# Optimization experiments

Hardware: AMD Instinct MI355X
Metric: run time of the kernel (lower is better)

## Reference

```python
import jax, jax.numpy as jnp
import numpy as np

ALPHA = 0.2  # LeakyReLU negative slope from init kwarg
NEG_INF = -9e15


def gat_multihead(x, adj_mask, W, a, concat):
    """Standard (GLMP-style) dense GAT, all heads at once.
    x: [B,N,Din], adj_mask: [B,N,N] bool, W: [H,Din,F], a: [H,2F].
    """
    B, N, _ = x.shape
    H, _, F = W.shape
    Wh = jnp.einsum('bnd,hdf->bhnf', x, W)              # [B,H,N,F]
    f1 = jnp.einsum('bhnf,hf->bhn', Wh, a[:, :F])
    f2 = jnp.einsum('bhnf,hf->bhn', Wh, a[:, F:])
    e = jax.nn.leaky_relu(f1[:, :, :, None] + f2[:, :, None, :], ALPHA)  # [B,H,N,N]
    e = jnp.where(adj_mask[:, None], e, NEG_INF)
    att = jax.nn.softmax(e, axis=-1)
    out = jnp.einsum('bhij,bhjf->bhif', att, Wh)        # [B,H,N,F]
    if concat:
        out = jax.nn.elu(out)
        return out.transpose(0, 2, 1, 3).reshape(B, N, H * F)
    # concat=False heads are summed and divided by nheads in load_graph -> mean
    return out.mean(axis=1)


def setup_inputs() -> dict:
    key = jax.random.key(0)
    ks = jax.random.split(key, 12)
    B, N, T = 16, 1024, 6
    V, D, F, H = 32000, 128, 64, 4
    CONV_MAX = 400
    story = jax.random.randint(ks[0], (B, N, T), 0, V)
    kb_len = jax.random.randint(ks[1], (B,), 1, CONV_MAX)
    conv_len = jax.random.randint(ks[2], (B,), 1, CONV_MAX)
    hidden = jax.random.normal(ks[3], (B, F), dtype=jnp.float32)
    dh_outputs = jax.random.normal(ks[4], (B, CONV_MAX, D), dtype=jnp.float32)
    adj = (jax.random.uniform(ks[5], (B, N, N)) < 0.05).astype(jnp.float32)
    emb = jax.random.normal(ks[6], (V, D), dtype=jnp.float32) * 0.1
    W1 = jax.random.normal(ks[7], (H, D, F), dtype=jnp.float32) * 0.1
    a1 = jax.random.normal(ks[8], (H, 2 * F), dtype=jnp.float32) * 0.1
    W2 = jax.random.normal(ks[9], (H, H * F, F), dtype=jnp.float32) * 0.1
    a2 = jax.random.normal(ks[10], (H, 2 * F), dtype=jnp.float32) * 0.1
    W3 = jax.random.normal(ks[11], (H, H * F, F), dtype=jnp.float32) * 0.1
    a3 = jax.random.normal(jax.random.fold_in(key, 99), (H, 2 * F), dtype=jnp.float32) * 0.1
    return {"story": story, "kb_len": kb_len, "conv_len": conv_len,
            "hidden": hidden, "dh_outputs": dh_outputs, "adj": adj,
            "emb": emb, "W1": W1, "a1": a1, "W2": W2, "a2": a2, "W3": W3, "a3": a3}


def reference(story, kb_len, conv_len, hidden, dh_outputs, adj, emb, W1, a1, W2, a2, W3, a3):
    B, N, T = story.shape
    Lc = dh_outputs.shape[1]
    # Embedding lookup + bag-of-words sum over memory token slots
    x = emb[story].sum(axis=2)                              # [B,N,D]
    # add_lm_embedding: scatter dh_outputs[b, :conv_len[b]] into slots
    # [kb_len[b]-1, kb_len[b]-1+conv_len[b]) of the memory (vectorized)
    pos = jnp.arange(N)[None, :]                            # [1,N]
    off = pos - (kb_len[:, None] - 1)                       # [B,N]
    valid = (off >= 0) & (off < conv_len[:, None])
    idx = jnp.clip(off, 0, Lc - 1)
    gathered = jnp.take_along_axis(dh_outputs, idx[:, :, None], axis=1)  # [B,N,D]
    x = x + jnp.where(valid[:, :, None], gathered, 0.0)
    # update_pad_token_adj: self-loop for pad slots k >= kb_len+conv_len
    d = jnp.arange(N)
    start = kb_len + conv_len                               # (kb_len-1)+conv_len+1
    diag = adj[:, d, d]
    adj = adj.at[:, d, d].set(jnp.where(d[None, :] >= start[:, None], 1.0, diag))
    adj_mask = adj > 0
    # Three GAT stacks (dropout omitted: eval mode)
    x = gat_multihead(x, adj_mask, W1, a1, concat=True)     # [B,N,H*F]
    x = gat_multihead(x, adj_mask, W2, a2, concat=True)     # [B,N,H*F]
    x = jax.nn.sigmoid(gat_multihead(x, adj_mask, W3, a3, concat=False))  # [B,N,F]
    prob_logits = jnp.einsum('bnf,bf->bn', x, hidden)       # [B,N]
    return (jax.nn.sigmoid(prob_logits), hidden, prob_logits)
```

## Files before the change

### kernel.cpp

```cpp
#include <hip/hip_runtime.h>
#include <stdint.h>

typedef short bf16x8 __attribute__((ext_vector_type(8)));
typedef float f32x4 __attribute__((ext_vector_type(4)));
typedef unsigned short u16;
typedef unsigned short u16x4 __attribute__((ext_vector_type(4)));
typedef unsigned int u32;
typedef unsigned int u32x4 __attribute__((ext_vector_type(4)));
typedef unsigned long long u64;


__device__ inline u16 f2b(float f) {
    unsigned u = __float_as_uint(f);
    u += 0x7fffu + ((u >> 16) & 1u);
    return (u16)(u >> 16);
}

__device__ inline float wred_sum(float v) {
    #pragma unroll
    for (int m = 32; m >= 1; m >>= 1) v += __shfl_xor(v, m, 64);
    return v;
}

__global__ __launch_bounds__(256) void k_pre(const float* __restrict__ adj,
                                             const int* __restrict__ kb,
                                             const int* __restrict__ cv,
                                             const int* __restrict__ story,
                                             const float* __restrict__ dh,
                                             const float* __restrict__ emb,
                                             const float* __restrict__ W1,
                                             const float* __restrict__ a1,
                                             const float* __restrict__ W2,
                                             const float* __restrict__ a2,
                                             const float* __restrict__ W3,
                                             const float* __restrict__ a3,
                                             u64* __restrict__ mask,
                                             u16* __restrict__ x0,
                                             u16* __restrict__ Bp1,
                                             u16* __restrict__ Bp2,
                                             u16* __restrict__ Bp3,
                                             float* __restrict__ d0g) {
    int bid = blockIdx.x;
    int tid = threadIdx.x;
    if (bid < 1024) {
        int w = tid >> 6, l = tid & 63;
        int rbase = (bid << 4) + (w << 2);
        int b = rbase >> 10;
        int start = kb[b] + cv[b];
        const float4* a4 = (const float4*)adj;
        for (int r = 0; r < 4; ++r) {
            int row = rbase + r;
            int i = row & 1023;
            u32 m16 = 0;
            #pragma unroll
            for (int q = 0; q < 4; ++q) {
                float4 v = a4[(size_t)row * 256 + (l << 2) + q];
                m16 |= (u32)(v.x > 0.0f) << (q * 4);
                m16 |= (u32)(v.y > 0.0f) << (q * 4 + 1);
                m16 |= (u32)(v.z > 0.0f) << (q * 4 + 2);
                m16 |= (u32)(v.w > 0.0f) << (q * 4 + 3);
            }
            if (i >= start && (i >> 4) == l) m16 |= 1u << (i & 15);
            u64 bal = __ballot(m16 != 0);
            u32 s0 = (u32)__shfl((int)m16, (l << 2) + 0, 64);
            u32 s1 = (u32)__shfl((int)m16, (l << 2) + 1, 64);
            u32 s2 = (u32)__shfl((int)m16, (l << 2) + 2, 64);
            u32 s3 = (u32)__shfl((int)m16, (l << 2) + 3, 64);
            if (l < 16) {
                u64 word = (u64)(s0 | (s1 << 16)) | ((u64)(s2 | (s3 << 16)) << 32);
                mask[((size_t)row << 4) + l] = word;
            }
            if (l == 0) d0g[row] = (bal == 0ull) ? 1.0f : 0.0f;
        }
    } else if (bid < 3072) {
        int w = tid >> 6, l = tid & 63;
        int r = l >> 5, dq = l & 31;
        int bn = ((bid - 1024) << 3) + (w << 1) + r;
        int b = bn >> 10, n = bn & 1023;
        const int* st = story + (size_t)bn * 6;
        const float4* emb4 = (const float4*)emb;
        float4 acc = {0.f, 0.f, 0.f, 0.f};
        #pragma unroll
        for (int t = 0; t < 6; ++t) {
            int tok = st[t];
            float4 e = emb4[(size_t)tok * 32 + dq];
            acc.x += e.x; acc.y += e.y; acc.z += e.z; acc.w += e.w;
        }
        int off = n - (kb[b] - 1);
        if (off >= 0 && off < cv[b]) {
            float4 d = ((const float4*)dh)[((size_t)b * 400 + off) * 32 + dq];
            acc.x += d.x; acc.y += d.y; acc.z += d.z; acc.w += d.w;
        }
        u16x4 pk = {f2b(acc.x), f2b(acc.y), f2b(acc.z), f2b(acc.w)};
        *(u16x4*)(x0 + ((size_t)bn << 7) + (dq << 2)) = pk;
    } else {
        int pb = bid - 3072;
        const float *W, *a; u16* Bp; int K;
        if (pb < 136)      { W = W1; a = a1; Bp = Bp1; K = 128; }
        else if (pb < 408) { W = W2; a = a2; Bp = Bp2; K = 256; pb -= 136; }
        else               { W = W3; a = a3; Bp = Bp3; K = 256; pb -= 408; }
        int id = pb * 256 + tid;
        int j = id & 7, lane = (id >> 3) & 63, fr = id >> 9;
        int kt = fr / 17, ct = fr - kt * 17;
        int kk = (kt << 5) + ((lane >> 4) << 3) + j;
        u16 o;
        if (ct < 16) {
            int col = (ct << 4) | (lane & 15);
            o = f2b(W[((size_t)(col >> 6) * K + kk) * 64 + (col & 63)]);
        } else {
            int c = lane & 15;
            if (c < 8) {
                int h = c >> 1, wh = c & 1;
                const float4* wr = (const float4*)(W + ((size_t)h * K + kk) * 64);
                const float4* av = (const float4*)(a + h * 128 + wh * 64);
                float s = 0.0f;
                #pragma unroll
                for (int q = 0; q < 16; ++q) {
                    float4 x = wr[q], y = av[q];
                    s += x.x * y.x + x.y * y.y + x.z * y.z + x.w * y.w;
                }
                o = f2b(s);
            } else o = 0;
        }
        Bp[id] = o;
    }
}

template <int KT>
__global__ __launch_bounds__(256) void k_gemm(const u16* __restrict__ A,
                                              const u16* __restrict__ Bp,
                                              u16* __restrict__ WhB,
                                              float* __restrict__ f1,
                                              float* __restrict__ f2) {
    constexpr int K = KT * 32;
    __shared__ __align__(16) u16 tile[4][2][2048];
    int tid = threadIdx.x, w = tid >> 6, l = tid & 63;
    int rtp = blockIdx.x;
    int colq = w;
    int m0 = rtp << 5;
    int b = m0 >> 10, n0 = m0 & 1023;
    int jt = n0 >> 5;
    const bf16x8* Av = (const bf16x8*)A;
    const bf16x8* Bv = (const bf16x8*)Bp;
    int arowA = m0 + (l & 15);
    bf16x8 afA[KT], afB[KT];
    #pragma unroll
    for (int kt = 0; kt < KT; ++kt) {
        size_t base = ((size_t)arowA * K + (kt << 5) + ((l >> 4) << 3)) >> 3;
        afA[kt] = Av[base];
        afB[kt] = Av[base + ((16 * K) >> 3)];
    }
    f32x4 accA[4], accB[4];
    #pragma unroll
    for (int c = 0; c < 4; ++c) { accA[c] = f32x4{0.f,0.f,0.f,0.f}; accB[c] = f32x4{0.f,0.f,0.f,0.f}; }
    f32x4 acc16A = {0.f,0.f,0.f,0.f}, acc16B = {0.f,0.f,0.f,0.f};
    #pragma unroll
    for (int kt = 0; kt < KT; ++kt) {
        #pragma unroll
        for (int c = 0; c < 4; ++c) {
            bf16x8 bv = Bv[(size_t)(kt * 17 + (colq << 2) + c) * 64 + l];
            accA[c] = __builtin_amdgcn_mfma_f32_16x16x32_bf16(afA[kt], bv, accA[c], 0, 0, 0);
            accB[c] = __builtin_amdgcn_mfma_f32_16x16x32_bf16(afB[kt], bv, accB[c], 0, 0, 0);
        }
        if (colq == 0) {
            bf16x8 bv = Bv[(size_t)(kt * 17 + 16) * 64 + l];
            acc16A = __builtin_amdgcn_mfma_f32_16x16x32_bf16(afA[kt], bv, acc16A, 0, 0, 0);
            acc16B = __builtin_amdgcn_mfma_f32_16x16x32_bf16(afB[kt], bv, acc16B, 0, 0, 0);
        }
    }
    int co = l & 15, ro = (l >> 4) << 2;
    if (colq == 0 && co < 8) {
        int hh = co >> 1;
        float* fp = (co & 1) ? f2 : f1;
        int base = (((b << 2) + hh) << 10) + n0 + ro;
        #pragma unroll
        for (int r = 0; r < 4; ++r) {
            fp[base + r] = acc16A[r];
            fp[base + 16 + r] = acc16B[r];
        }
    }
    u16* twA = tile[w][0]; u16* twB = tile[w][1];
    #pragma unroll
    for (int c = 0; c < 4; ++c) {
        int col2 = (c << 4) + co;
        u16x4 pkA, pkB;
        #pragma unroll
        for (int r = 0; r < 4; ++r) { pkA[r] = f2b(accA[c][r]); pkB[r] = f2b(accB[c][r]); }
        *(u16x4*)(twA + (col2 << 4) + ro) = pkA;
        *(u16x4*)(twB + (col2 << 4) + ro) = pkB;
    }
    __syncthreads();
    int bh = (b << 2) + colq;
    int lq = l & 31;
    #pragma unroll
    for (int ftq = 0; ftq < 2; ++ftq) {
        int ft = (ftq << 1) + (l >> 5);
        int col2 = (ft << 4) + (l & 15);
        int r0 = ((l >> 4) & 1) << 3;
        bf16x8 vA = *(const bf16x8*)(twA + (col2 << 4) + r0);
        bf16x8 vB = *(const bf16x8*)(twB + (col2 << 4) + r0);
        size_t fidx = (size_t)((bh << 7) + (jt << 2) + ft);
        *(bf16x8*)(WhB + (fidx * 64 + lq) * 8) = vA;
        *(bf16x8*)(WhB + (fidx * 64 + 32 + lq) * 8) = vB;
    }
}

#define PV_CORE(f2v4, mw, f1i, d0f, fragbase, Bv, acc, accs, g)                  \
    {                                                                            \
        u32 onep = ((l & 15) == 0) ? 0x3F803F80u : 0u;                           \
        u32x4 ov = {onep, onep, onep, onep};                                     \
        bf16x8 sfrag = __builtin_bit_cast(bf16x8, ov);                           \
        for (int jt = 0; jt < 32; ++jt) {                                        \
            u32 sh = mw[jt] >> (g << 3);                                         \
            f32x4 fa = f2v4[(jt << 3) + (g << 1)];                               \
            f32x4 fb = f2v4[(jt << 3) + (g << 1) + 1];                           \
            float p[8];                                                          \
            _Pragma("unroll")                                                    \
            for (int jj = 0; jj < 8; ++jj) {                                     \
                float f2j = (jj < 4) ? fa[jj] : fb[jj - 4];                      \
                float t = f1i + f2j;                                             \
                float e = fmaxf(t, 0.2f * t);                                    \
                float ex;                                                        \
                asm("v_exp_f32 %0, %1" : "=v"(ex) : "v"(e));                     \
                p[jj] = (sh & (1u << jj)) ? ex : d0f;                            \
            }                                                                    \
            u32x4 pk;                                                            \
            _Pragma("unroll")                                                    \
            for (int q = 0; q < 4; ++q) {                                        \
                u32 r;                                                           \
                asm("v_cvt_pk_bf16_f32 %0, %1, %2"                               \
                    : "=v"(r) : "v"(p[2 * q]), "v"(p[2 * q + 1]));               \
                pk[q] = r;                                                       \
            }                                                                    \
            bf16x8 af = __builtin_bit_cast(bf16x8, pk);                          \
            accs = __builtin_amdgcn_mfma_f32_16x16x32_bf16(af, sfrag, accs, 0, 0, 0); \
            _Pragma("unroll")                                                    \
            for (int ft = 0; ft < 4; ++ft)                                       \
                acc[ft] = __builtin_amdgcn_mfma_f32_16x16x32_bf16(               \
                    af, Bv[(size_t)(fragbase + (jt << 2) + ft) * 64 + l], acc[ft], 0, 0, 0); \
        }                                                                        \
    }

__global__ __launch_bounds__(256) void k_pv0(const u32* __restrict__ mask32,
                                             const float* __restrict__ f1g,
                                             const float* __restrict__ f2g,
                                             const float* __restrict__ d0g,
                                             const bf16x8* __restrict__ Bv,
                                             u16* __restrict__ xout) {
    __shared__ __align__(16) float f2s[1024];
    const float LOG2E = 1.44269504088896340736f;
    int tid = threadIdx.x;
    int w = tid >> 6, l = tid & 63;
    int bh = blockIdx.x >> 4;
    int b = bh >> 2, h = bh & 3;
    int itile = ((blockIdx.x & 15) << 2) + w;
    int i0 = itile << 4;
    for (int idx = tid; idx < 1024; idx += 256) f2s[idx] = f2g[(bh << 10) + idx] * LOG2E;
    __syncthreads();
    int row = l & 15, g = l >> 4;
    int i = i0 + row;
    float f1i = f1g[(bh << 10) + i] * LOG2E;
    float d0f = d0g[(b << 10) + i];
    const u32x4* m4 = (const u32x4*)(mask32 + (((size_t)(b << 10) + i) << 5));
    u32 mw[32];
    #pragma unroll
    for (int t4 = 0; t4 < 8; ++t4) {
        u32x4 q = m4[t4];
        mw[t4 * 4 + 0] = q[0]; mw[t4 * 4 + 1] = q[1];
        mw[t4 * 4 + 2] = q[2]; mw[t4 * 4 + 3] = q[3];
    }
    f32x4 acc[4];
    #pragma unroll
    for (int ft = 0; ft < 4; ++ft) acc[ft] = f32x4{0.f, 0.f, 0.f, 0.f};
    f32x4 accs = {0.f, 0.f, 0.f, 0.f};
    const f32x4* f2v4 = (const f32x4*)f2s;
    int fragbase = bh << 7;
    PV_CORE(f2v4, mw, f1i, d0f, fragbase, Bv, acc, accs, g)
    #pragma unroll
    for (int reg = 0; reg < 4; ++reg) {
        int orow = (g << 2) + reg;
        float s = __shfl(accs[reg], g << 4, 64);
        float rinv = 1.0f / s;
        int grow = i0 + orow;
        #pragma unroll
        for (int ft = 0; ft < 4; ++ft) {
            float v = acc[ft][reg] * rinv;
            float e2 = v > 0.0f ? v : (__expf(v) - 1.0f);
            xout[((size_t)((b << 10) + grow) << 8) + (h << 6) + (ft << 4) + row] = f2b(e2);
        }
    }
}

__global__ __launch_bounds__(256) void k_pv3(const u32* __restrict__ mask32,
                                             const float* __restrict__ f1g,
                                             const float* __restrict__ f2g,
                                             const float* __restrict__ d0g,
                                             const bf16x8* __restrict__ Bv,
                                             const float* __restrict__ hidden,
                                             float* __restrict__ dout) {
    __shared__ __align__(16) float shbuf[4096];
    const float LOG2E = 1.44269504088896340736f;
    int tid = threadIdx.x;
    int w = tid >> 6, l = tid & 63;
    int b = blockIdx.x >> 6;
    int itile = blockIdx.x & 63;
    int i0 = itile << 4;
    int bh = (b << 2) + w;
    for (int idx = tid; idx < 4096; idx += 256) shbuf[idx] = f2g[(b << 12) + idx] * LOG2E;
    __syncthreads();
    int row = l & 15, g = l >> 4;
    int i = i0 + row;
    float f1i = f1g[(bh << 10) + i] * LOG2E;
    float d0f = d0g[(b << 10) + i];
    const u32x4* m4 = (const u32x4*)(mask32 + (((size_t)(b << 10) + i) << 5));
    u32 mw[32];
    #pragma unroll
    for (int t4 = 0; t4 < 8; ++t4) {
        u32x4 q = m4[t4];
        mw[t4 * 4 + 0] = q[0]; mw[t4 * 4 + 1] = q[1];
        mw[t4 * 4 + 2] = q[2]; mw[t4 * 4 + 3] = q[3];
    }
    f32x4 acc[4];
    #pragma unroll
    for (int ft = 0; ft < 4; ++ft) acc[ft] = f32x4{0.f, 0.f, 0.f, 0.f};
    f32x4 accs = {0.f, 0.f, 0.f, 0.f};
    const f32x4* f2v4 = (const f32x4*)(shbuf + (w << 10));
    int fragbase = bh << 7;
    PV_CORE(f2v4, mw, f1i, d0f, fragbase, Bv, acc, accs, g)
    __syncthreads();
    #pragma unroll
    for (int reg = 0; reg < 4; ++reg) {
        int orow = (g << 2) + reg;
        float s = __shfl(accs[reg], g << 4, 64);
        float rinv = 1.0f / s;
        #pragma unroll
        for (int ft = 0; ft < 4; ++ft)
            shbuf[(w << 10) + (orow << 6) + (ft << 4) + row] = acc[ft][reg] * rinv;
    }
    __syncthreads();
    float hid = hidden[(b << 6) + l];
    #pragma unroll
    for (int k = 0; k < 4; ++k) {
        int rl = (k << 2) + w;
        int o = (rl << 6) + l;
        float s = shbuf[o] + shbuf[1024 + o] + shbuf[2048 + o] + shbuf[3072 + o];
        s *= 0.25f;
        float x = 1.0f / (1.0f + __expf(-s));
        float logit = wred_sum(x * hid);
        if (l == 0) {
            int grow = i0 + rl;
            dout[(b << 10) + grow] = 1.0f / (1.0f + __expf(-logit));
            dout[17408 + (b << 10) + grow] = logit;
        }
    }
    if (itile == 0 && w == 0) dout[16384 + (b << 6) + l] = hid;
}

extern "C" void kernel_launch(void* const* d_in, const int* in_sizes, int n_in,
                              void* d_out, int out_size, void* d_ws, size_t ws_size,
                              hipStream_t stream) {
    const int*   story  = (const int*)d_in[0];
    const int*   kb     = (const int*)d_in[1];
    const int*   cv     = (const int*)d_in[2];
    const float* hidden = (const float*)d_in[3];
    const float* dh     = (const float*)d_in[4];
    const float* adj    = (const float*)d_in[5];
    const float* emb    = (const float*)d_in[6];
    const float* W1     = (const float*)d_in[7];
    const float* a1     = (const float*)d_in[8];
    const float* W2     = (const float*)d_in[9];
    const float* a2     = (const float*)d_in[10];
    const float* W3     = (const float*)d_in[11];
    const float* a3     = (const float*)d_in[12];
    float* dout = (float*)d_out;

    char* ws = (char*)d_ws;
    u64*   mask   = (u64*)(ws + 0);
    u32*   mask32 = (u32*)(ws + 0);
    u16*   x0   = (u16*)(ws + 2097152);
    u16*   xbf  = (u16*)(ws + 6291456);
    u16*   WhB  = (u16*)(ws + 14680064);
    float* f1   = (float*)(ws + 23068672);
    float* f2   = (float*)(ws + 23330816);
    u16*   Bp1  = (u16*)(ws + 23592960);
    u16*   Bp2  = (u16*)(ws + 23662592);
    u16*   Bp3  = (u16*)(ws + 23801856);
    float* d0g  = (float*)(ws + 23941120);

    k_pre<<<3752, 256, 0, stream>>>(adj, kb, cv, story, dh, emb,
                                    W1, a1, W2, a2, W3, a3,
                                    mask, x0, Bp1, Bp2, Bp3, d0g);

    k_gemm<4><<<512, 256, 0, stream>>>(x0, Bp1, WhB, f1, f2);
    k_pv0<<<1024, 256, 0, stream>>>(mask32, f1, f2, d0g, (const bf16x8*)WhB, xbf);

    k_gemm<8><<<512, 256, 0, stream>>>(xbf, Bp2, WhB, f1, f2);
    k_pv0<<<1024, 256, 0, stream>>>(mask32, f1, f2, d0g, (const bf16x8*)WhB, xbf);

    k_gemm<8><<<512, 256, 0, stream>>>(xbf, Bp3, WhB, f1, f2);
    k_pv3<<<1024, 256, 0, stream>>>(mask32, f1, f2, d0g, (const bf16x8*)WhB, hidden, dout);
}
```

Baseline: 151.5 us.

## Halve GEMM row tile and split final layer into PV plus reduction kernel

The projection GEMM now processes 16 rows per block instead of 32, doubling the grid to 1024 blocks and dropping the block-wide barrier. The last attention layer reuses the generic PV kernel to write per-head fp32 outputs to workspace, and a new kernel averages the heads, applies the sigmoid and computes the logits. The aim is more parallelism in the GEMM and a PV kernel that is lighter on shared memory and needs fewer barriers. The cost is an extra launch and an fp32 round-trip through global memory for the final layer, and each GEMM block now reloads the B fragments for half as many rows.

```diff
diff --git a/kernel.cpp b/kernel.cpp
--- a/kernel.cpp
+++ b/kernel.cpp
@@ -133,40 +133,33 @@
                                               float* __restrict__ f1,
                                               float* __restrict__ f2) {
     constexpr int K = KT * 32;
-    __shared__ __align__(16) u16 tile[4][2][2048];
+    __shared__ __align__(16) u16 tile[4][1024];
     int tid = threadIdx.x, w = tid >> 6, l = tid & 63;
-    int rtp = blockIdx.x;
     int colq = w;
-    int m0 = rtp << 5;
+    int m0 = blockIdx.x << 4;
     int b = m0 >> 10, n0 = m0 & 1023;
-    int jt = n0 >> 5;
+    int jt = n0 >> 5, halfsel = (n0 >> 4) & 1;
     const bf16x8* Av = (const bf16x8*)A;
     const bf16x8* Bv = (const bf16x8*)Bp;
-    int arowA = m0 + (l & 15);
-    bf16x8 afA[KT], afB[KT];
-    #pragma unroll
-    for (int kt = 0; kt < KT; ++kt) {
-        size_t base = ((size_t)arowA * K + (kt << 5) + ((l >> 4) << 3)) >> 3;
-        afA[kt] = Av[base];
-        afB[kt] = Av[base + ((16 * K) >> 3)];
-    }
-    f32x4 accA[4], accB[4];
-    #pragma unroll
-    for (int c = 0; c < 4; ++c) { accA[c] = f32x4{0.f,0.f,0.f,0.f}; accB[c] = f32x4{0.f,0.f,0.f,0.f}; }
-    f32x4 acc16A = {0.f,0.f,0.f,0.f}, acc16B = {0.f,0.f,0.f,0.f};
+    int arow = m0 + (l & 15);
+    bf16x8 af[KT];
+    #pragma unroll
+    for (int kt = 0; kt < KT; ++kt)
+        af[kt] = Av[((size_t)arow * K + (kt << 5) + ((l >> 4) << 3)) >> 3];
+    f32x4 acc[4];
+    #pragma unroll
+    for (int c = 0; c < 4; ++c) acc[c] = f32x4{0.f, 0.f, 0.f, 0.f};
+    f32x4 acc16 = {0.f, 0.f, 0.f, 0.f};
     #pragma unroll
     for (int kt = 0; kt < KT; ++kt) {
         #pragma unroll
         for (int c = 0; c < 4; ++c) {
             bf16x8 bv = Bv[(size_t)(kt * 17 + (colq << 2) + c) * 64 + l];
-            accA[c] = __builtin_amdgcn_mfma_f32_16x16x32_bf16(afA[kt], bv, accA[c], 0, 0, 0);
-            accB[c] = __builtin_amdgcn_mfma_f32_16x16x32_bf16(afB[kt], bv, accB[c], 0, 0, 0);
-        }
-        if (colq == 0) {
-            bf16x8 bv = Bv[(size_t)(kt * 17 + 16) * 64 + l];
-            acc16A = __builtin_amdgcn_mfma_f32_16x16x32_bf16(afA[kt], bv, acc16A, 0, 0, 0);
-            acc16B = __builtin_amdgcn_mfma_f32_16x16x32_bf16(afB[kt], bv, acc16B, 0, 0, 0);
-        }
+            acc[c] = __builtin_amdgcn_mfma_f32_16x16x32_bf16(af[kt], bv, acc[c], 0, 0, 0);
+        }
+        if (colq == 0)
+            acc16 = __builtin_amdgcn_mfma_f32_16x16x32_bf16(
+                af[kt], Bv[(size_t)(kt * 17 + 16) * 64 + l], acc16, 0, 0, 0);
     }
     int co = l & 15, ro = (l >> 4) << 2;
     if (colq == 0 && co < 8) {
@@ -174,34 +167,27 @@
         float* fp = (co & 1) ? f2 : f1;
         int base = (((b << 2) + hh) << 10) + n0 + ro;
         #pragma unroll
-        for (int r = 0; r < 4; ++r) {
-            fp[base + r] = acc16A[r];
-            fp[base + 16 + r] = acc16B[r];
-        }
-    }
-    u16* twA = tile[w][0]; u16* twB = tile[w][1];
+        for (int r = 0; r < 4; ++r) fp[base + r] = acc16[r];
+    }
+    u16* tw = tile[w];
     #pragma unroll
     for (int c = 0; c < 4; ++c) {
         int col2 = (c << 4) + co;
-        u16x4 pkA, pkB;
-        #pragma unroll
-        for (int r = 0; r < 4; ++r) { pkA[r] = f2b(accA[c][r]); pkB[r] = f2b(accB[c][r]); }
-        *(u16x4*)(twA + (col2 << 4) + ro) = pkA;
-        *(u16x4*)(twB + (col2 << 4) + ro) = pkB;
-    }
-    __syncthreads();
+        u16x4 pk;
+        #pragma unroll
+        for (int r = 0; r < 4; ++r) pk[r] = f2b(acc[c][r]);
+        *(u16x4*)(tw + (col2 << 4) + ro) = pk;
+    }
     int bh = (b << 2) + colq;
-    int lq = l & 31;
+    int lp = (halfsel << 5) + (l & 31);
     #pragma unroll
     for (int ftq = 0; ftq < 2; ++ftq) {
         int ft = (ftq << 1) + (l >> 5);
         int col2 = (ft << 4) + (l & 15);
         int r0 = ((l >> 4) & 1) << 3;
-        bf16x8 vA = *(const bf16x8*)(twA + (col2 << 4) + r0);
-        bf16x8 vB = *(const bf16x8*)(twB + (col2 << 4) + r0);
+        bf16x8 v = *(const bf16x8*)(tw + (col2 << 4) + r0);
         size_t fidx = (size_t)((bh << 7) + (jt << 2) + ft);
-        *(bf16x8*)(WhB + (fidx * 64 + lq) * 8) = vA;
-        *(bf16x8*)(WhB + (fidx * 64 + 32 + lq) * 8) = vB;
+        *(bf16x8*)(WhB + (fidx * 64 + lp) * 8) = v;
     }
 }
 
@@ -241,12 +227,14 @@
         }                                                                        \
     }
 
-__global__ __launch_bounds__(256) void k_pv0(const u32* __restrict__ mask32,
-                                             const float* __restrict__ f1g,
-                                             const float* __restrict__ f2g,
-                                             const float* __restrict__ d0g,
-                                             const bf16x8* __restrict__ Bv,
-                                             u16* __restrict__ xout) {
+template <int MODE>
+__global__ __launch_bounds__(256) void k_pv(const u32* __restrict__ mask32,
+                                            const float* __restrict__ f1g,
+                                            const float* __restrict__ f2g,
+                                            const float* __restrict__ d0g,
+                                            const bf16x8* __restrict__ Bv,
+                                            u16* __restrict__ xout,
+                                            float* __restrict__ out3) {
     __shared__ __align__(16) float f2s[1024];
     const float LOG2E = 1.44269504088896340736f;
     int tid = threadIdx.x;
@@ -285,75 +273,35 @@
         #pragma unroll
         for (int ft = 0; ft < 4; ++ft) {
             float v = acc[ft][reg] * rinv;
-            float e2 = v > 0.0f ? v : (__expf(v) - 1.0f);
-            xout[((size_t)((b << 10) + grow) << 8) + (h << 6) + (ft << 4) + row] = f2b(e2);
-        }
-    }
-}
-
-__global__ __launch_bounds__(256) void k_pv3(const u32* __restrict__ mask32,
-                                             const float* __restrict__ f1g,
-                                             const float* __restrict__ f2g,
-                                             const float* __restrict__ d0g,
-                                             const bf16x8* __restrict__ Bv,
-                                             const float* __restrict__ hidden,
-                                             float* __restrict__ dout) {
-    __shared__ __align__(16) float shbuf[4096];
-    const float LOG2E = 1.44269504088896340736f;
-    int tid = threadIdx.x;
-    int w = tid >> 6, l = tid & 63;
-    int b = blockIdx.x >> 6;
-    int itile = blockIdx.x & 63;
-    int i0 = itile << 4;
-    int bh = (b << 2) + w;
-    for (int idx = tid; idx < 4096; idx += 256) shbuf[idx] = f2g[(b << 12) + idx] * LOG2E;
-    __syncthreads();
-    int row = l & 15, g = l >> 4;
-    int i = i0 + row;
-    float f1i = f1g[(bh << 10) + i] * LOG2E;
-    float d0f = d0g[(b << 10) + i];
-    const u32x4* m4 = (const u32x4*)(mask32 + (((size_t)(b << 10) + i) << 5));
-    u32 mw[32];
-    #pragma unroll
-    for (int t4 = 0; t4 < 8; ++t4) {
-        u32x4 q = m4[t4];
-        mw[t4 * 4 + 0] = q[0]; mw[t4 * 4 + 1] = q[1];
-        mw[t4 * 4 + 2] = q[2]; mw[t4 * 4 + 3] = q[3];
-    }
-    f32x4 acc[4];
-    #pragma unroll
-    for (int ft = 0; ft < 4; ++ft) acc[ft] = f32x4{0.f, 0.f, 0.f, 0.f};
-    f32x4 accs = {0.f, 0.f, 0.f, 0.f};
-    const f32x4* f2v4 = (const f32x4*)(shbuf + (w << 10));
-    int fragbase = bh << 7;
-    PV_CORE(f2v4, mw, f1i, d0f, fragbase, Bv, acc, accs, g)
-    __syncthreads();
-    #pragma unroll
-    for (int reg = 0; reg < 4; ++reg) {
-        int orow = (g << 2) + reg;
-        float s = __shfl(accs[reg], g << 4, 64);
-        float rinv = 1.0f / s;
-        #pragma unroll
-        for (int ft = 0; ft < 4; ++ft)
-            shbuf[(w << 10) + (orow << 6) + (ft << 4) + row] = acc[ft][reg] * rinv;
-    }
-    __syncthreads();
-    float hid = hidden[(b << 6) + l];
-    #pragma unroll
-    for (int k = 0; k < 4; ++k) {
-        int rl = (k << 2) + w;
-        int o = (rl << 6) + l;
-        float s = shbuf[o] + shbuf[1024 + o] + shbuf[2048 + o] + shbuf[3072 + o];
-        s *= 0.25f;
-        float x = 1.0f / (1.0f + __expf(-s));
-        float logit = wred_sum(x * hid);
-        if (l == 0) {
-            int grow = i0 + rl;
-            dout[(b << 10) + grow] = 1.0f / (1.0f + __expf(-logit));
-            dout[17408 + (b << 10) + grow] = logit;
-        }
-    }
-    if (itile == 0 && w == 0) dout[16384 + (b << 6) + l] = hid;
+            if (MODE == 0) {
+                float e2 = v > 0.0f ? v : (__expf(v) - 1.0f);
+                xout[((size_t)((b << 10) + grow) << 8) + (h << 6) + (ft << 4) + row] = f2b(e2);
+            } else {
+                out3[((size_t)((bh << 10) + grow) << 6) + (ft << 4) + row] = v;
+            }
+        }
+    }
+}
+
+__global__ __launch_bounds__(256) void k_final(const float* __restrict__ out3,
+                                               const float* __restrict__ hidden,
+                                               float* __restrict__ dout) {
+    int tid = threadIdx.x, w = tid >> 6, f = tid & 63;
+    int bn = blockIdx.x * 4 + w;
+    int b = bn >> 10, n = bn & 1023;
+    float s = 0.0f;
+    #pragma unroll
+    for (int h = 0; h < 4; ++h)
+        s += out3[((size_t)((((b << 2) + h) << 10) + n) << 6) + f];
+    s *= 0.25f;
+    float x = 1.0f / (1.0f + __expf(-s));
+    float hid = hidden[(b << 6) + f];
+    float logit = wred_sum(x * hid);
+    if (f == 0) {
+        dout[bn] = 1.0f / (1.0f + __expf(-logit));
+        dout[17408 + bn] = logit;
+    }
+    if (n == 0) dout[16384 + (b << 6) + f] = hid;
 }
 
 extern "C" void kernel_launch(void* const* d_in, const int* in_sizes, int n_in,
@@ -386,17 +334,20 @@
     u16*   Bp2  = (u16*)(ws + 23662592);
     u16*   Bp3  = (u16*)(ws + 23801856);
     float* d0g  = (float*)(ws + 23941120);
+    float* out3 = (float*)(ws + 25165824);
 
     k_pre<<<3752, 256, 0, stream>>>(adj, kb, cv, story, dh, emb,
                                     W1, a1, W2, a2, W3, a3,
                                     mask, x0, Bp1, Bp2, Bp3, d0g);
 
-    k_gemm<4><<<512, 256, 0, stream>>>(x0, Bp1, WhB, f1, f2);
-    k_pv0<<<1024, 256, 0, stream>>>(mask32, f1, f2, d0g, (const bf16x8*)WhB, xbf);
-
-    k_gemm<8><<<512, 256, 0, stream>>>(xbf, Bp2, WhB, f1, f2);
-    k_pv0<<<1024, 256, 0, stream>>>(mask32, f1, f2, d0g, (const bf16x8*)WhB, xbf);
-
-    k_gemm<8><<<512, 256, 0, stream>>>(xbf, Bp3, WhB, f1, f2);
-    k_pv3<<<1024, 256, 0, stream>>>(mask32, f1, f2, d0g, (const bf16x8*)WhB, hidden, dout);
-}
+    k_gemm<4><<<1024, 256, 0, stream>>>(x0, Bp1, WhB, f1, f2);
+    k_pv<0><<<1024, 256, 0, stream>>>(mask32, f1, f2, d0g, (const bf16x8*)WhB, xbf, nullptr);
+
+    k_gemm<8><<<1024, 256, 0, stream>>>(xbf, Bp2, WhB, f1, f2);
+    k_pv<0><<<1024, 256, 0, stream>>>(mask32, f1, f2, d0g, (const bf16x8*)WhB, xbf, nullptr);
+
+    k_gemm<8><<<1024, 256, 0, stream>>>(xbf, Bp3, WhB, f1, f2);
+    k_pv<1><<<1024, 256, 0, stream>>>(mask32, f1, f2, d0g, (const bf16x8*)WhB, nullptr, out3);
+
+    k_final<<<4096, 256, 0, stream>>>(out3, hidden, dout);
+}
```

Result: slower. 155.8 us (+2.9%).

## Split k_pv0 key dimension across two waves and combine partial sums in LDS

Applied to the files above, without the earlier changes.

Each row tile of k_pv0 is now handled by two waves, each covering half of the 1024 key columns, which doubles the grid to 2048 blocks. The second wave writes its partial P·V and row-sum accumulators to shared memory, and the first wave adds them before normalising and applying ELU. Mask words are loaded incrementally instead of being held as a full 32-register array, and launch bounds request 8 blocks per CU. The aim is more parallelism and lower register pressure, at the cost of an extra LDS reduction, a block-wide sync, and half the waves idling during the epilogue.

```diff
diff --git a/kernel.cpp b/kernel.cpp
--- a/kernel.cpp
+++ b/kernel.cpp
@@ -241,19 +241,21 @@
         }                                                                        \
     }
 
-__global__ __launch_bounds__(256) void k_pv0(const u32* __restrict__ mask32,
-                                             const float* __restrict__ f1g,
-                                             const float* __restrict__ f2g,
-                                             const float* __restrict__ d0g,
-                                             const bf16x8* __restrict__ Bv,
-                                             u16* __restrict__ xout) {
+__global__ __launch_bounds__(256, 8) void k_pv0(const u32* __restrict__ mask32,
+                                                const float* __restrict__ f1g,
+                                                const float* __restrict__ f2g,
+                                                const float* __restrict__ d0g,
+                                                const bf16x8* __restrict__ Bv,
+                                                u16* __restrict__ xout) {
     __shared__ __align__(16) float f2s[1024];
+    __shared__ float comb[2][20][64];
     const float LOG2E = 1.44269504088896340736f;
     int tid = threadIdx.x;
     int w = tid >> 6, l = tid & 63;
-    int bh = blockIdx.x >> 4;
+    int bh = blockIdx.x >> 5;
     int b = bh >> 2, h = bh & 3;
-    int itile = ((blockIdx.x & 15) << 2) + w;
+    int slot = w >> 1, jh = w & 1;
+    int itile = ((blockIdx.x & 31) << 1) + slot;
     int i0 = itile << 4;
     for (int idx = tid; idx < 1024; idx += 256) f2s[idx] = f2g[(bh << 10) + idx] * LOG2E;
     __syncthreads();
@@ -261,32 +263,74 @@
     int i = i0 + row;
     float f1i = f1g[(bh << 10) + i] * LOG2E;
     float d0f = d0g[(b << 10) + i];
-    const u32x4* m4 = (const u32x4*)(mask32 + (((size_t)(b << 10) + i) << 5));
-    u32 mw[32];
-    #pragma unroll
-    for (int t4 = 0; t4 < 8; ++t4) {
-        u32x4 q = m4[t4];
-        mw[t4 * 4 + 0] = q[0]; mw[t4 * 4 + 1] = q[1];
-        mw[t4 * 4 + 2] = q[2]; mw[t4 * 4 + 3] = q[3];
-    }
+    const u32x4* m4 = (const u32x4*)(mask32 + (((size_t)(b << 10) + i) << 5)) + (jh << 2);
     f32x4 acc[4];
     #pragma unroll
     for (int ft = 0; ft < 4; ++ft) acc[ft] = f32x4{0.f, 0.f, 0.f, 0.f};
     f32x4 accs = {0.f, 0.f, 0.f, 0.f};
     const f32x4* f2v4 = (const f32x4*)f2s;
     int fragbase = bh << 7;
-    PV_CORE(f2v4, mw, f1i, d0f, fragbase, Bv, acc, accs, g)
-    #pragma unroll
-    for (int reg = 0; reg < 4; ++reg) {
-        int orow = (g << 2) + reg;
-        float s = __shfl(accs[reg], g << 4, 64);
-        float rinv = 1.0f / s;
-        int grow = i0 + orow;
-        #pragma unroll
-        for (int ft = 0; ft < 4; ++ft) {
-            float v = acc[ft][reg] * rinv;
-            float e2 = v > 0.0f ? v : (__expf(v) - 1.0f);
-            xout[((size_t)((b << 10) + grow) << 8) + (h << 6) + (ft << 4) + row] = f2b(e2);
+    {
+        u32 onep = (row == 0) ? 0x3F803F80u : 0u;
+        u32x4 ov = {onep, onep, onep, onep};
+        bf16x8 sfrag = __builtin_bit_cast(bf16x8, ov);
+        u32x4 mwq;
+        for (int t = 0; t < 16; ++t) {
+            if ((t & 3) == 0) mwq = m4[t >> 2];
+            int jtg = (jh << 4) + t;
+            u32 sh = mwq[t & 3] >> (g << 3);
+            f32x4 fa = f2v4[(jtg << 3) + (g << 1)];
+            f32x4 fb = f2v4[(jtg << 3) + (g << 1) + 1];
+            float p[8];
+            #pragma unroll
+            for (int jj = 0; jj < 8; ++jj) {
+                float f2j = (jj < 4) ? fa[jj] : fb[jj - 4];
+                float tt = f1i + f2j;
+                float e = fmaxf(tt, 0.2f * tt);
+                float ex;
+                asm("v_exp_f32 %0, %1" : "=v"(ex) : "v"(e));
+                p[jj] = (sh & (1u << jj)) ? ex : d0f;
+            }
+            u32x4 pk;
+            #pragma unroll
+            for (int q = 0; q < 4; ++q) {
+                u32 r;
+                asm("v_cvt_pk_bf16_f32 %0, %1, %2"
+                    : "=v"(r) : "v"(p[2 * q]), "v"(p[2 * q + 1]));
+                pk[q] = r;
+            }
+            bf16x8 af = __builtin_bit_cast(bf16x8, pk);
+            accs = __builtin_amdgcn_mfma_f32_16x16x32_bf16(af, sfrag, accs, 0, 0, 0);
+            #pragma unroll
+            for (int ft = 0; ft < 4; ++ft)
+                acc[ft] = __builtin_amdgcn_mfma_f32_16x16x32_bf16(
+                    af, Bv[(size_t)(fragbase + (jtg << 2) + ft) * 64 + l], acc[ft], 0, 0, 0);
+        }
+    }
+    if (jh == 1) {
+        #pragma unroll
+        for (int v = 0; v < 16; ++v) comb[slot][v][l] = acc[v >> 2][v & 3];
+        #pragma unroll
+        for (int r = 0; r < 4; ++r) comb[slot][16 + r][l] = accs[r];
+    }
+    __syncthreads();
+    if (jh == 0) {
+        #pragma unroll
+        for (int v = 0; v < 16; ++v) acc[v >> 2][v & 3] += comb[slot][v][l];
+        #pragma unroll
+        for (int r = 0; r < 4; ++r) accs[r] += comb[slot][16 + r][l];
+        #pragma unroll
+        for (int reg = 0; reg < 4; ++reg) {
+            int orow = (g << 2) + reg;
+            float s = __shfl(accs[reg], g << 4, 64);
+            float rinv = 1.0f / s;
+            int grow = i0 + orow;
+            #pragma unroll
+            for (int ft = 0; ft < 4; ++ft) {
+                float v = acc[ft][reg] * rinv;
+                float e2 = v > 0.0f ? v : (__expf(v) - 1.0f);
+                xout[((size_t)((b << 10) + grow) << 8) + (h << 6) + (ft << 4) + row] = f2b(e2);
+            }
         }
     }
 }
@@ -392,10 +436,10 @@
                                     mask, x0, Bp1, Bp2, Bp3, d0g);
 
     k_gemm<4><<<512, 256, 0, stream>>>(x0, Bp1, WhB, f1, f2);
-    k_pv0<<<1024, 256, 0, stream>>>(mask32, f1, f2, d0g, (const bf16x8*)WhB, xbf);
+    k_pv0<<<2048, 256, 0, stream>>>(mask32, f1, f2, d0g, (const bf16x8*)WhB, xbf);
 
     k_gemm<8><<<512, 256, 0, stream>>>(xbf, Bp2, WhB, f1, f2);
-    k_pv0<<<1024, 256, 0, stream>>>(mask32, f1, f2, d0g, (const bf16x8*)WhB, xbf);
+    k_pv0<<<2048, 256, 0, stream>>>(mask32, f1, f2, d0g, (const bf16x8*)WhB, xbf);
 
     k_gemm<8><<<512, 256, 0, stream>>>(xbf, Bp3, WhB, f1, f2);
     k_pv3<<<1024, 256, 0, stream>>>(mask32, f1, f2, d0g, (const bf16x8*)WhB, hidden, dout);
```

Measured after the change: 143.9 us. 1.05x faster.
